# Optimization experiments

Measured on AMD Instinct MI355X. Metric: run time of the kernel, lower is better.

The kernel has to match this reference:

```python
import jax, jax.numpy as jnp
import numpy as np

N, E = 100000, 1600000
DIMS = [128, 64, 64, 64, 32]  # in, hid, hid, hid, out
NEG_SLOPE = 0.2               # GATv2Conv default negative_slope
ELU_ALPHA_OUT = float(DIMS[-1])  # nn.ELU(out_channels): alpha = out_channels


def setup_inputs() -> dict:
    key = jax.random.key(0)
    ks = jax.random.split(key, 16)
    inp = {
        "x": jax.random.normal(ks[0], (N, DIMS[0]), dtype=jnp.float32),
        "edge_index": jax.random.randint(ks[1], (2, E), 0, N, dtype=jnp.int64),
    }
    ki = 2
    for i in range(4):
        fin, fout = DIMS[i], DIMS[i + 1]
        s = 1.0 / np.sqrt(fin)
        inp[f"Wl{i+1}"] = jax.random.uniform(ks[ki], (fin, fout), jnp.float32, -s, s); ki += 1
        inp[f"Wr{i+1}"] = jax.random.uniform(ks[ki], (fin, fout), jnp.float32, -s, s); ki += 1
        inp[f"att{i+1}"] = jax.random.uniform(ks[ki], (fout,), jnp.float32, -s, s); ki += 1
    return inp


def gatv2_layer(x, src, dst, Wl, Wr, att):
    # single head, concat=False, no self-loops, no bias (per module config)
    xl = x @ Wl                                   # [N, F] source-side projection
    xr = x @ Wr                                   # [N, F] target-side projection
    e = jax.nn.leaky_relu(xl[src] + xr[dst], NEG_SLOPE)   # [E, F]
    score = e @ att                               # [E]
    # softmax over incoming edges of each destination node
    m = jax.ops.segment_max(score, dst, num_segments=N)    # [N]
    ex = jnp.exp(score - m[dst])                  # [E]
    denom = jax.ops.segment_sum(ex, dst, num_segments=N)   # [N]
    alpha = ex / (denom[dst] + 1e-16)             # [E]
    # scatter-add weighted source messages
    return jax.ops.segment_sum(xl[src] * alpha[:, None], dst, num_segments=N)


def reference(x, edge_index, Wl1, Wr1, att1, Wl2, Wr2, att2, Wl3, Wr3, att3, Wl4, Wr4, att4):
    src, dst = edge_index[0], edge_index[1]
    h = jax.nn.elu(gatv2_layer(x, src, dst, Wl1, Wr1, att1))
    h = jax.nn.elu(gatv2_layer(h, src, dst, Wl2, Wr2, att2))
    h = jax.nn.elu(gatv2_layer(h, src, dst, Wl3, Wr3, att3))
    h = gatv2_layer(h, src, dst, Wl4, Wr4, att4)
    # nn.ELU(out_channels) -> ELU with alpha = out_channels (faithful quirk)
    return jnp.where(h > 0, h, ELU_ALPHA_OUT * jnp.expm1(h))
```

## Files before the change

### kernel.cpp

```cpp
#include <hip/hip_runtime.h>
#include <math.h>

typedef __attribute__((ext_vector_type(8))) short bf16x8;
typedef __attribute__((ext_vector_type(4))) float f32x4;
typedef __attribute__((ext_vector_type(2))) _Float16 h2;

#define BSHIFT 7
#define CH 8192

__device__ inline unsigned short f32_to_bf16_bits(float f) {
    unsigned int u = __float_as_uint(f);
    unsigned int r = (u + 0x7fffu + ((u >> 16) & 1u)) >> 16;
    return (unsigned short)r;
}
__device__ inline float bf16_bits_to_f32(unsigned short h) {
    return __uint_as_float(((unsigned int)h) << 16);
}
__device__ inline h2 u2h(unsigned u) { return __builtin_bit_cast(h2, u); }
__device__ inline unsigned h2u(h2 h) { return __builtin_bit_cast(unsigned, h); }

#define SWZ_ADD(t, imm) \
    t += __int_as_float(__builtin_amdgcn_ds_swizzle(__float_as_int(t), imm))

__device__ inline float dot2acc(h2 a, h2 b, float c) {
#if defined(__has_builtin)
#if __has_builtin(__builtin_amdgcn_fdot2)
    return __builtin_amdgcn_fdot2(a, b, c, false);
#else
    return c + (float)a[0] * (float)b[0] + (float)a[1] * (float)b[1];
#endif
#else
    return c + (float)a[0] * (float)b[0] + (float)a[1] * (float)b[1];
#endif
}


__global__ __launch_bounds__(256) void bucket_hist(
    const int* __restrict__ dst, int* __restrict__ bcnt8, int E, int nb, int nbp)
{
    __shared__ int h[1024];
    for (int i = threadIdx.x; i < nb; i += 256) h[i] = 0;
    __syncthreads();
    int e0 = blockIdx.x * CH, e1 = min(e0 + CH, E);
    for (int e = e0 + (int)threadIdx.x; e < e1; e += 256)
        atomicAdd(&h[dst[e] >> BSHIFT], 1);
    __syncthreads();
    int* mycnt = bcnt8 + (blockIdx.x & 7) * nbp;
    for (int b = threadIdx.x; b < nb; b += 256) {
        int c = h[b];
        if (c) atomicAdd(&mycnt[b], c);
    }
}

__global__ void bucket_scan(const int* __restrict__ bcnt8, int* __restrict__ bbase,
                            int* __restrict__ bcur8, int* __restrict__ rowstart,
                            int nb, int nbp, int E, int N)
{
    __shared__ int sh[1024];
    int t = threadIdx.x;
    int g8[8];
    int tot = 0;
#pragma unroll
    for (int g = 0; g < 8; ++g) {
        int c = (t < nb) ? bcnt8[g * nbp + t] : 0;
        g8[g] = c; tot += c;
    }
    sh[t] = tot;
    __syncthreads();
    for (int d = 1; d < 1024; d <<= 1) {
        int a = (t >= d) ? sh[t - d] : 0;
        __syncthreads();
        sh[t] += a;
        __syncthreads();
    }
    int base = sh[t] - tot;
    if (t <= nb) bbase[t] = base;
    if (t < nb) {
        int run = base;
#pragma unroll
        for (int g = 0; g < 8; ++g) { bcur8[g * nbp + t] = run; run += g8[g]; }
    }
    if (t == 0) rowstart[N] = E;
}

__global__ __launch_bounds__(256) void bucket_scatter(
    const int* __restrict__ src, const int* __restrict__ dst,
    int* __restrict__ bcur8, unsigned* __restrict__ pairs, int E, int nb, int nbp)
{
    __shared__ int h[1024];
    for (int i = threadIdx.x; i < nb; i += 256) h[i] = 0;
    __syncthreads();
    int e0 = blockIdx.x * CH, e1 = min(e0 + CH, E);
    for (int e = e0 + (int)threadIdx.x; e < e1; e += 256)
        atomicAdd(&h[dst[e] >> BSHIFT], 1);
    __syncthreads();
    int* mycur = bcur8 + (blockIdx.x & 7) * nbp;
    for (int b = threadIdx.x; b < nb; b += 256) {
        int c = h[b];
        if (c) h[b] = atomicAdd(&mycur[b], c);
    }
    __syncthreads();
    for (int e = e0 + (int)threadIdx.x; e < e1; e += 256) {
        int d = dst[e];
        int pos = atomicAdd(&h[d >> BSHIFT], 1);
        pairs[pos] = ((unsigned)src[e] << BSHIFT) | (unsigned)(d & 127);
    }
}

__global__ __launch_bounds__(256) void bucket_finalize(
    const unsigned* __restrict__ pairs, const int* __restrict__ bbase,
    int* __restrict__ rowstart, int* __restrict__ csr_src, int N)
{
    __shared__ int h[128];
    __shared__ int sh[256];
    int b = blockIdx.x;
    int p0 = bbase[b], p1 = bbase[b + 1];
    int t = threadIdx.x;
    if (t < 128) h[t] = 0;
    __syncthreads();
    for (int e = p0 + t; e < p1; e += 256)
        atomicAdd(&h[pairs[e] & 127], 1);
    __syncthreads();
    int v = (t < 128) ? h[t] : 0;
    sh[t] = v;
    __syncthreads();
    for (int d = 1; d < 256; d <<= 1) {
        int a = (t >= d) ? sh[t - d] : 0;
        __syncthreads();
        sh[t] += a;
        __syncthreads();
    }
    if (t < 128) {
        int off = sh[t] - v;
        int node = (b << BSHIFT) + t;
        if (node < N) rowstart[node] = p0 + off;
        h[t] = p0 + off;
    }
    __syncthreads();
    for (int e = p0 + t; e < p1; e += 256) {
        unsigned pr = pairs[e];
        int pos = atomicAdd(&h[pr & 127], 1);
        csr_src[pos] = (int)(pr >> BSHIFT);
    }
}


__global__ void prepack_kernel(const float* __restrict__ Wl, const float* __restrict__ Wr,
                               unsigned short* __restrict__ pWl, unsigned short* __restrict__ pWr,
                               int FIN, int FOUT) {
    int NT = FOUT >> 4, NK = FIN >> 5;
    int part = NT * NK * 512;
    int i = blockIdx.x * blockDim.x + threadIdx.x;
    int m = i / part;
    if (m >= 2) return;
    int ii = i - m * part;
    int j = ii & 7;
    int lane = (ii >> 3) & 63;
    int rest = ii >> 9;
    int ks = rest % NK;
    int t = rest / NK;
    int k = ks * 32 + (lane >> 4) * 8 + j;
    int c = t * 16 + (lane & 15);
    const float* W = m ? Wr : Wl;
    unsigned short* P = m ? pWr : pWl;
    float w = W[(size_t)k * FOUT + c];
    unsigned short hi = f32_to_bf16_bits(w);
    unsigned short lo = f32_to_bf16_bits(w - bf16_bits_to_f32(hi));
    P[ii] = hi;
    P[part + ii] = lo;
}


template<int FIN, int FOUT>
__global__ __launch_bounds__(256) void proj_mfma_kernel(
    const float* __restrict__ x,
    const unsigned short* __restrict__ pWl, const unsigned short* __restrict__ pWr,
    const float* __restrict__ att,
    _Float16* __restrict__ xlh, _Float16* __restrict__ xrh,
    float* __restrict__ dl, float* __restrict__ dr, int n)
{
    constexpr int NT = FOUT >> 4;
    constexpr int NK = FIN >> 5;
    constexpr int PART = NT * NK * 512;
    const int wave = threadIdx.x >> 6;
    const int lane = threadIdx.x & 63;
    const int row0 = blockIdx.x * 64 + wave * 16;
    int arow = row0 + (lane & 15);
    if (arow >= n) arow = n - 1;
    const int khalf = lane >> 4;

    f32x4 accl[NT], accr[NT];
#pragma unroll
    for (int t = 0; t < NT; ++t) {
        accl[t] = (f32x4){0.f, 0.f, 0.f, 0.f};
        accr[t] = (f32x4){0.f, 0.f, 0.f, 0.f};
    }

    const float* xrow = x + (size_t)arow * FIN + khalf * 8;
#pragma unroll
    for (int ks = 0; ks < NK; ++ks) {
        float4 a0 = *(const float4*)(xrow + ks * 32);
        float4 a1 = *(const float4*)(xrow + ks * 32 + 4);
        float av[8] = {a0.x, a0.y, a0.z, a0.w, a1.x, a1.y, a1.z, a1.w};
        bf16x8 ah, al;
#pragma unroll
        for (int j = 0; j < 8; ++j) {
            unsigned short h = f32_to_bf16_bits(av[j]);
            ah[j] = (short)h;
            al[j] = (short)f32_to_bf16_bits(av[j] - bf16_bits_to_f32(h));
        }
#pragma unroll
        for (int t = 0; t < NT; ++t) {
            const unsigned short* bpl = pWl + ((size_t)(t * NK + ks) * 64 + lane) * 8;
            bf16x8 bh  = *(const bf16x8*)bpl;
            bf16x8 blo = *(const bf16x8*)(bpl + PART);
            accl[t] = __builtin_amdgcn_mfma_f32_16x16x32_bf16(ah, bh,  accl[t], 0, 0, 0);
            accl[t] = __builtin_amdgcn_mfma_f32_16x16x32_bf16(ah, blo, accl[t], 0, 0, 0);
            accl[t] = __builtin_amdgcn_mfma_f32_16x16x32_bf16(al, bh,  accl[t], 0, 0, 0);
            const unsigned short* bpr = pWr + ((size_t)(t * NK + ks) * 64 + lane) * 8;
            bh  = *(const bf16x8*)bpr;
            blo = *(const bf16x8*)(bpr + PART);
            accr[t] = __builtin_amdgcn_mfma_f32_16x16x32_bf16(ah, bh,  accr[t], 0, 0, 0);
            accr[t] = __builtin_amdgcn_mfma_f32_16x16x32_bf16(ah, blo, accr[t], 0, 0, 0);
            accr[t] = __builtin_amdgcn_mfma_f32_16x16x32_bf16(al, bh,  accr[t], 0, 0, 0);
        }
    }

    const int orow0 = row0 + khalf * 4;
    const int colb = lane & 15;
    float attc[NT];
#pragma unroll
    for (int t = 0; t < NT; ++t) attc[t] = att[t * 16 + colb];

#pragma unroll
    for (int t = 0; t < NT; ++t) {
        int col = t * 16 + colb;
#pragma unroll
        for (int r = 0; r < 4; ++r) {
            int rr = orow0 + r;
            if (rr < n) {
                xlh[(size_t)rr * FOUT + col] = (_Float16)accl[t][r];
                xrh[(size_t)rr * FOUT + col] = (_Float16)accr[t][r];
            }
        }
    }
#pragma unroll
    for (int r = 0; r < 4; ++r) {
        float pl = 0.f, pr = 0.f;
#pragma unroll
        for (int t = 0; t < NT; ++t) { pl += accl[t][r] * attc[t]; pr += accr[t][r] * attc[t]; }
#pragma unroll
        for (int off = 1; off < 16; off <<= 1) {
            pl += __shfl_xor(pl, off);
            pr += __shfl_xor(pr, off);
        }
        int rr = orow0 + r;
        if (colb == 0 && rr < n) { dl[rr] = pl; dr[rr] = pr; }
    }
}


template<int F, int AMODE>
__global__ __launch_bounds__(256) void agg_kernel(
    const _Float16* __restrict__ xlh, const _Float16* __restrict__ xrh,
    const float* __restrict__ att,
    const float* __restrict__ dl, const float* __restrict__ dr,
    const int* __restrict__ rowstart, const int* __restrict__ csr_src,
    float* __restrict__ out, int n, int E)
{
    constexpr int LPE = F / 8;
    constexpr int LSH = (F == 64) ? 6 : 5;
    constexpr int NPG = 64 / LPE;

    int wv  = (blockIdx.x * blockDim.x + threadIdx.x) >> 6;
    int lane = threadIdx.x & 63;
    int grp = lane / LPE;
    int fl  = lane % LPE;
    int node = wv * NPG + grp;
    bool act = node < n;
    int nc = act ? node : 0;

    float4 xrraw = *(const float4*)(xrh + (((unsigned)nc << LSH) + fl * 8));
    h2 xrv[4];
#pragma unroll
    for (int j = 0; j < 4; ++j) xrv[j] = u2h(((const unsigned*)&xrraw)[j]);
    h2 atth[4];
#pragma unroll
    for (int j = 0; j < 4; ++j) {
        atth[j][0] = (_Float16)att[fl * 8 + 2 * j];
        atth[j][1] = (_Float16)att[fl * 8 + 2 * j + 1];
    }
    float cdr = 0.6f * dr[nc];

    int s0 = rowstart[nc];
    int s1 = act ? rowstart[nc + 1] : s0;
    int s1c = min(max(s1 - 1, s0), E - 1);

    float m = -1e30f, mth = -1e30f, ssum = 0.f;
    float o[8];
#pragma unroll
    for (int j = 0; j < 8; ++j) o[j] = 0.f;

    int cA0 = csr_src[min(s0,     s1c)];
    int cB0 = csr_src[min(s0 + 1, s1c)];
    int cA1 = csr_src[min(s0 + 2, s1c)];
    int cB1 = csr_src[min(s0 + 3, s1c)];
    float4 rA0 = *(const float4*)(xlh + (((unsigned)cA0 << LSH) + fl * 8));
    float4 rB0 = *(const float4*)(xlh + (((unsigned)cB0 << LSH) + fl * 8));
    float  dA0 = dl[cA0], dB0 = dl[cB0];
    float4 rA1 = *(const float4*)(xlh + (((unsigned)cA1 << LSH) + fl * 8));
    float4 rB1 = *(const float4*)(xlh + (((unsigned)cB1 << LSH) + fl * 8));
    float  dA1 = dl[cA1], dB1 = dl[cB1];
    int fA0 = csr_src[min(s0 + 4, s1c)];
    int fB0 = csr_src[min(s0 + 5, s1c)];
    int fA1 = csr_src[min(s0 + 6, s1c)];
    int fB1 = csr_src[min(s0 + 7, s1c)];

    int i0 = s0;

#define AGG_COMPUTE(RA, RB, DA, DB)                                          \
    {                                                                        \
        h2 a[4], b[4];                                                       \
        _Pragma("unroll")                                                    \
        for (int j = 0; j < 4; ++j) {                                        \
            a[j] = u2h(((const unsigned*)&RA)[j]);                           \
            b[j] = u2h(((const unsigned*)&RB)[j]);                           \
        }                                                                    \
        bool vb = (i0 + 1) < s1;                                             \
        float ta = 0.f, tb = 0.f;                                            \
        _Pragma("unroll")                                                    \
        for (int j = 0; j < 4; ++j) {                                        \
            h2 ea = a[j] + xrv[j];                                           \
            h2 eb = b[j] + xrv[j];                                           \
            ea = u2h(h2u(ea) & 0x7FFF7FFFu);                                 \
            eb = u2h(h2u(eb) & 0x7FFF7FFFu);                                 \
            ta = dot2acc(atth[j], ea, ta);                                   \
            tb = dot2acc(atth[j], eb, tb);                                   \
        }                                                                    \
        SWZ_ADD(ta, 0x041F); SWZ_ADD(tb, 0x041F);                            \
        SWZ_ADD(ta, 0x081F); SWZ_ADD(tb, 0x081F);                            \
        if (LPE == 8) { SWZ_ADD(ta, 0x101F); SWZ_ADD(tb, 0x101F); }          \
        float pa = 0.6f * DA + cdr + 0.4f * ta;                              \
        float pb = vb ? (0.6f * DB + cdr + 0.4f * tb) : -1e30f;              \
        float pm = fmaxf(pa, pb);                                            \
        if (pm > mth) {                                                      \
            float c = __expf(m - pm);                                        \
            ssum *= c;                                                       \
            _Pragma("unroll")                                                \
            for (int j = 0; j < 8; ++j) o[j] *= c;                           \
            m = pm; mth = pm + 8.0f;                                         \
        }                                                                    \
        float wa = __expf(pa - m);                                           \
        float wb = __expf(pb - m);                                           \
        ssum += wa + wb;                                                     \
        _Pragma("unroll")                                                    \
        for (int j = 0; j < 4; ++j) {                                        \
            o[2 * j]     += wa * (float)a[j][0] + wb * (float)b[j][0];       \
            o[2 * j + 1] += wa * (float)a[j][1] + wb * (float)b[j][1];       \
        }                                                                    \
    }

    while (i0 < s1) {
        {
            int cA2 = fA0, cB2 = fB0;
            fA0 = csr_src[min(i0 + 8, s1c)];
            fB0 = csr_src[min(i0 + 9, s1c)];
            AGG_COMPUTE(rA0, rB0, dA0, dB0);
            rA0 = *(const float4*)(xlh + (((unsigned)cA2 << LSH) + fl * 8));
            rB0 = *(const float4*)(xlh + (((unsigned)cB2 << LSH) + fl * 8));
            dA0 = dl[cA2]; dB0 = dl[cB2];
        }
        i0 += 2;
        if (i0 >= s1) break;
        {
            int cA2 = fA1, cB2 = fB1;
            fA1 = csr_src[min(i0 + 8, s1c)];
            fB1 = csr_src[min(i0 + 9, s1c)];
            AGG_COMPUTE(rA1, rB1, dA1, dB1);
            rA1 = *(const float4*)(xlh + (((unsigned)cA2 << LSH) + fl * 8));
            rB1 = *(const float4*)(xlh + (((unsigned)cB2 << LSH) + fl * 8));
            dA1 = dl[cA2]; dB1 = dl[cB2];
        }
        i0 += 2;
    }
#undef AGG_COMPUTE

    float inv = 1.f / (ssum + 1e-16f);
    float res[8];
#pragma unroll
    for (int j = 0; j < 8; ++j) {
        float r = o[j] * inv;
        if (AMODE == 1) r = (r > 0.f) ? r : expm1f(r);
        else            r = (r > 0.f) ? r : 32.f * expm1f(r);
        res[j] = r;
    }
    if (act) {
        float* op = out + (((unsigned)node << LSH) + fl * 8);
        *(float4*)op       = (float4){res[0], res[1], res[2], res[3]};
        *(float4*)(op + 4) = (float4){res[4], res[5], res[6], res[7]};
    }
}


extern "C" void kernel_launch(void* const* d_in, const int* in_sizes, int n_in,
                              void* d_out, int out_size, void* d_ws, size_t ws_size,
                              hipStream_t stream) {
    const float* x    = (const float*)d_in[0];
    const int*   ei   = (const int*)d_in[1];
    const float* Wl1  = (const float*)d_in[2];
    const float* Wr1  = (const float*)d_in[3];
    const float* att1 = (const float*)d_in[4];
    const float* Wl2  = (const float*)d_in[5];
    const float* Wr2  = (const float*)d_in[6];
    const float* att2 = (const float*)d_in[7];
    const float* Wl3  = (const float*)d_in[8];
    const float* Wr3  = (const float*)d_in[9];
    const float* att3 = (const float*)d_in[10];
    const float* Wl4  = (const float*)d_in[11];
    const float* Wr4  = (const float*)d_in[12];
    const float* att4 = (const float*)d_in[13];

    const int N = in_sizes[0] / 128;
    const int E = in_sizes[1] / 2;
    const int* src = ei;
    const int* dst = ei + E;

    const int nb  = (N + 127) >> BSHIFT;
    const int nbp = (nb + 15) & ~15;

    char* w = (char*)d_ws;
    size_t off = 0;
    auto take = [&](size_t bytes) -> void* {
        void* p = w + off;
        off = (off + bytes + 255) & ~(size_t)255;
        return p;
    };
    int* bcnt8    = (int*)take((size_t)8 * nbp * 4);
    int* bcur8    = (int*)take((size_t)8 * nbp * 4);
    int* bbase    = (int*)take((size_t)(nb + 1) * 4);
    int* rowstart = (int*)take((size_t)(N + 1) * 4);
    int* csr_src  = (int*)take((size_t)E * 4);
    float* dl = (float*)take((size_t)N * 4);
    float* dr = (float*)take((size_t)N * 4);
    _Float16* xlh = (_Float16*)take((size_t)N * 64 * 2);
    _Float16* xrh = (_Float16*)take((size_t)N * 64 * 2);
    float* hA = (float*)take((size_t)N * 64 * 4);
    float* hB = (float*)take((size_t)N * 64 * 4);
    unsigned short* pWl1 = (unsigned short*)take(2 * 4 * 4 * 512 * 2);
    unsigned short* pWr1 = (unsigned short*)take(2 * 4 * 4 * 512 * 2);
    unsigned short* pWl2 = (unsigned short*)take(2 * 4 * 2 * 512 * 2);
    unsigned short* pWr2 = (unsigned short*)take(2 * 4 * 2 * 512 * 2);
    unsigned short* pWl3 = (unsigned short*)take(2 * 4 * 2 * 512 * 2);
    unsigned short* pWr3 = (unsigned short*)take(2 * 4 * 2 * 512 * 2);
    unsigned short* pWl4 = (unsigned short*)take(2 * 2 * 2 * 512 * 2);
    unsigned short* pWr4 = (unsigned short*)take(2 * 2 * 2 * 512 * 2);
    unsigned* pairs = (unsigned*)hA;
    float* outf = (float*)d_out;

    hipMemsetAsync(bcnt8, 0, (size_t)8 * nbp * 4, stream);

    prepack_kernel<<<(2 * 4 * 4 * 512 + 255) / 256, 256, 0, stream>>>(Wl1, Wr1, pWl1, pWr1, 128, 64);
    prepack_kernel<<<(2 * 4 * 2 * 512 + 255) / 256, 256, 0, stream>>>(Wl2, Wr2, pWl2, pWr2, 64, 64);
    prepack_kernel<<<(2 * 4 * 2 * 512 + 255) / 256, 256, 0, stream>>>(Wl3, Wr3, pWl3, pWr3, 64, 64);
    prepack_kernel<<<(2 * 2 * 2 * 512 + 255) / 256, 256, 0, stream>>>(Wl4, Wr4, pWl4, pWr4, 64, 32);

    int kgrid = (E + CH - 1) / CH;
    bucket_hist<<<kgrid, 256, 0, stream>>>(dst, bcnt8, E, nb, nbp);
    bucket_scan<<<1, 1024, 0, stream>>>(bcnt8, bbase, bcur8, rowstart, nb, nbp, E, N);
    bucket_scatter<<<kgrid, 256, 0, stream>>>(src, dst, bcur8, pairs, E, nb, nbp);
    bucket_finalize<<<nb, 256, 0, stream>>>(pairs, bbase, rowstart, csr_src, N);

    int pblk = (N + 63) / 64;
    int agg64 = (N + 31) / 32;
    int agg32 = (N + 63) / 64;

    proj_mfma_kernel<128, 64><<<pblk, 256, 0, stream>>>(x, pWl1, pWr1, att1, xlh, xrh, dl, dr, N);
    agg_kernel<64, 1><<<agg64, 256, 0, stream>>>(xlh, xrh, att1, dl, dr, rowstart, csr_src, hA, N, E);

    proj_mfma_kernel<64, 64><<<pblk, 256, 0, stream>>>(hA, pWl2, pWr2, att2, xlh, xrh, dl, dr, N);
    agg_kernel<64, 1><<<agg64, 256, 0, stream>>>(xlh, xrh, att2, dl, dr, rowstart, csr_src, hB, N, E);

    proj_mfma_kernel<64, 64><<<pblk, 256, 0, stream>>>(hB, pWl3, pWr3, att3, xlh, xrh, dl, dr, N);
    agg_kernel<64, 1><<<agg64, 256, 0, stream>>>(xlh, xrh, att3, dl, dr, rowstart, csr_src, hA, N, E);

    proj_mfma_kernel<64, 32><<<pblk, 256, 0, stream>>>(hA, pWl4, pWr4, att4, xlh, xrh, dl, dr, N);
    agg_kernel<32, 2><<<agg32, 256, 0, stream>>>(xlh, xrh, att4, dl, dr, rowstart, csr_src, outf, N, E);
}
```

Baseline: 295.5 us.

## Store hidden activations in fp16 and make aggregation grid-stride persistent

Intermediate layer outputs hA/hB are now written as fp16 by the aggregation kernel and read as fp16 by the next projection kernel. This halves activation write and read traffic. The aggregation kernel also becomes a persistent grid-stride loop over node tiles with a fixed grid of 1024 blocks, in place of one wave per tile. The fp16 activations add rounding error, and the persistent loop could change load balance and latency hiding.

```diff
diff --git a/kernel.cpp b/kernel.cpp
--- a/kernel.cpp
+++ b/kernel.cpp
@@ -171,9 +171,9 @@
 }
 
 
-template<int FIN, int FOUT>
+template<int FIN, int FOUT, bool IN16>
 __global__ __launch_bounds__(256) void proj_mfma_kernel(
-    const float* __restrict__ x,
+    const void* __restrict__ xin,
     const unsigned short* __restrict__ pWl, const unsigned short* __restrict__ pWr,
     const float* __restrict__ att,
     _Float16* __restrict__ xlh, _Float16* __restrict__ xrh,
@@ -196,12 +196,26 @@
         accr[t] = (f32x4){0.f, 0.f, 0.f, 0.f};
     }
 
-    const float* xrow = x + (size_t)arow * FIN + khalf * 8;
 #pragma unroll
     for (int ks = 0; ks < NK; ++ks) {
-        float4 a0 = *(const float4*)(xrow + ks * 32);
-        float4 a1 = *(const float4*)(xrow + ks * 32 + 4);
-        float av[8] = {a0.x, a0.y, a0.z, a0.w, a1.x, a1.y, a1.z, a1.w};
+        float av[8];
+        if (IN16) {
+            const _Float16* xrow = (const _Float16*)xin + (size_t)arow * FIN + khalf * 8;
+            float4 raw = *(const float4*)(xrow + ks * 32);
+            const unsigned* u = (const unsigned*)&raw;
+#pragma unroll
+            for (int j = 0; j < 4; ++j) {
+                h2 p = u2h(u[j]);
+                av[2 * j]     = (float)p[0];
+                av[2 * j + 1] = (float)p[1];
+            }
+        } else {
+            const float* xrow = (const float*)xin + (size_t)arow * FIN + khalf * 8;
+            float4 a0 = *(const float4*)(xrow + ks * 32);
+            float4 a1 = *(const float4*)(xrow + ks * 32 + 4);
+            av[0] = a0.x; av[1] = a0.y; av[2] = a0.z; av[3] = a0.w;
+            av[4] = a1.x; av[5] = a1.y; av[6] = a1.z; av[7] = a1.w;
+        }
         bf16x8 ah, al;
 #pragma unroll
         for (int j = 0; j < 8; ++j) {
@@ -260,144 +274,162 @@
 }
 
 
-template<int F, int AMODE>
+template<int F, int AMODE, bool OUT16>
 __global__ __launch_bounds__(256) void agg_kernel(
     const _Float16* __restrict__ xlh, const _Float16* __restrict__ xrh,
     const float* __restrict__ att,
     const float* __restrict__ dl, const float* __restrict__ dr,
     const int* __restrict__ rowstart, const int* __restrict__ csr_src,
-    float* __restrict__ out, int n, int E)
+    void* __restrict__ outv, int n, int E, int ntiles)
 {
     constexpr int LPE = F / 8;
     constexpr int LSH = (F == 64) ? 6 : 5;
     constexpr int NPG = 64 / LPE;
 
-    int wv  = (blockIdx.x * blockDim.x + threadIdx.x) >> 6;
+    int wv0  = (blockIdx.x * blockDim.x + threadIdx.x) >> 6;
+    int nwaves = gridDim.x * (blockDim.x >> 6);
     int lane = threadIdx.x & 63;
     int grp = lane / LPE;
     int fl  = lane % LPE;
-    int node = wv * NPG + grp;
-    bool act = node < n;
-    int nc = act ? node : 0;
-
-    float4 xrraw = *(const float4*)(xrh + (((unsigned)nc << LSH) + fl * 8));
-    h2 xrv[4];
-#pragma unroll
-    for (int j = 0; j < 4; ++j) xrv[j] = u2h(((const unsigned*)&xrraw)[j]);
+
     h2 atth[4];
 #pragma unroll
     for (int j = 0; j < 4; ++j) {
         atth[j][0] = (_Float16)att[fl * 8 + 2 * j];
         atth[j][1] = (_Float16)att[fl * 8 + 2 * j + 1];
     }
-    float cdr = 0.6f * dr[nc];
-
-    int s0 = rowstart[nc];
-    int s1 = act ? rowstart[nc + 1] : s0;
-    int s1c = min(max(s1 - 1, s0), E - 1);
-
-    float m = -1e30f, mth = -1e30f, ssum = 0.f;
-    float o[8];
-#pragma unroll
-    for (int j = 0; j < 8; ++j) o[j] = 0.f;
-
-    int cA0 = csr_src[min(s0,     s1c)];
-    int cB0 = csr_src[min(s0 + 1, s1c)];
-    int cA1 = csr_src[min(s0 + 2, s1c)];
-    int cB1 = csr_src[min(s0 + 3, s1c)];
-    float4 rA0 = *(const float4*)(xlh + (((unsigned)cA0 << LSH) + fl * 8));
-    float4 rB0 = *(const float4*)(xlh + (((unsigned)cB0 << LSH) + fl * 8));
-    float  dA0 = dl[cA0], dB0 = dl[cB0];
-    float4 rA1 = *(const float4*)(xlh + (((unsigned)cA1 << LSH) + fl * 8));
-    float4 rB1 = *(const float4*)(xlh + (((unsigned)cB1 << LSH) + fl * 8));
-    float  dA1 = dl[cA1], dB1 = dl[cB1];
-    int fA0 = csr_src[min(s0 + 4, s1c)];
-    int fB0 = csr_src[min(s0 + 5, s1c)];
-    int fA1 = csr_src[min(s0 + 6, s1c)];
-    int fB1 = csr_src[min(s0 + 7, s1c)];
-
-    int i0 = s0;
+
+    for (int tile = wv0; tile < ntiles; tile += nwaves) {
+        int node = tile * NPG + grp;
+        bool act = node < n;
+        int nc = act ? node : 0;
+
+        float4 xrraw = *(const float4*)(xrh + (((unsigned)nc << LSH) + fl * 8));
+        h2 xrv[4];
+#pragma unroll
+        for (int j = 0; j < 4; ++j) xrv[j] = u2h(((const unsigned*)&xrraw)[j]);
+        float cdr = 0.6f * dr[nc];
+
+        int s0 = rowstart[nc];
+        int s1 = act ? rowstart[nc + 1] : s0;
+        int s1c = min(max(s1 - 1, s0), E - 1);
+
+        float m = -1e30f, mth = -1e30f, ssum = 0.f;
+        float o[8];
+#pragma unroll
+        for (int j = 0; j < 8; ++j) o[j] = 0.f;
+
+        int cA0 = csr_src[min(s0,     s1c)];
+        int cB0 = csr_src[min(s0 + 1, s1c)];
+        int cA1 = csr_src[min(s0 + 2, s1c)];
+        int cB1 = csr_src[min(s0 + 3, s1c)];
+        float4 rA0 = *(const float4*)(xlh + (((unsigned)cA0 << LSH) + fl * 8));
+        float4 rB0 = *(const float4*)(xlh + (((unsigned)cB0 << LSH) + fl * 8));
+        float  dA0 = dl[cA0], dB0 = dl[cB0];
+        float4 rA1 = *(const float4*)(xlh + (((unsigned)cA1 << LSH) + fl * 8));
+        float4 rB1 = *(const float4*)(xlh + (((unsigned)cB1 << LSH) + fl * 8));
+        float  dA1 = dl[cA1], dB1 = dl[cB1];
+        int fA0 = csr_src[min(s0 + 4, s1c)];
+        int fB0 = csr_src[min(s0 + 5, s1c)];
+        int fA1 = csr_src[min(s0 + 6, s1c)];
+        int fB1 = csr_src[min(s0 + 7, s1c)];
+
+        int i0 = s0;
 
 #define AGG_COMPUTE(RA, RB, DA, DB)                                          \
-    {                                                                        \
-        h2 a[4], b[4];                                                       \
-        _Pragma("unroll")                                                    \
-        for (int j = 0; j < 4; ++j) {                                        \
-            a[j] = u2h(((const unsigned*)&RA)[j]);                           \
-            b[j] = u2h(((const unsigned*)&RB)[j]);                           \
-        }                                                                    \
-        bool vb = (i0 + 1) < s1;                                             \
-        float ta = 0.f, tb = 0.f;                                            \
-        _Pragma("unroll")                                                    \
-        for (int j = 0; j < 4; ++j) {                                        \
-            h2 ea = a[j] + xrv[j];                                           \
-            h2 eb = b[j] + xrv[j];                                           \
-            ea = u2h(h2u(ea) & 0x7FFF7FFFu);                                 \
-            eb = u2h(h2u(eb) & 0x7FFF7FFFu);                                 \
-            ta = dot2acc(atth[j], ea, ta);                                   \
-            tb = dot2acc(atth[j], eb, tb);                                   \
-        }                                                                    \
-        SWZ_ADD(ta, 0x041F); SWZ_ADD(tb, 0x041F);                            \
-        SWZ_ADD(ta, 0x081F); SWZ_ADD(tb, 0x081F);                            \
-        if (LPE == 8) { SWZ_ADD(ta, 0x101F); SWZ_ADD(tb, 0x101F); }          \
-        float pa = 0.6f * DA + cdr + 0.4f * ta;                              \
-        float pb = vb ? (0.6f * DB + cdr + 0.4f * tb) : -1e30f;              \
-        float pm = fmaxf(pa, pb);                                            \
-        if (pm > mth) {                                                      \
-            float c = __expf(m - pm);                                        \
-            ssum *= c;                                                       \
+        {                                                                    \
+            h2 a[4], b[4];                                                   \
             _Pragma("unroll")                                                \
-            for (int j = 0; j < 8; ++j) o[j] *= c;                           \
-            m = pm; mth = pm + 8.0f;                                         \
-        }                                                                    \
-        float wa = __expf(pa - m);                                           \
-        float wb = __expf(pb - m);                                           \
-        ssum += wa + wb;                                                     \
-        _Pragma("unroll")                                                    \
-        for (int j = 0; j < 4; ++j) {                                        \
-            o[2 * j]     += wa * (float)a[j][0] + wb * (float)b[j][0];       \
-            o[2 * j + 1] += wa * (float)a[j][1] + wb * (float)b[j][1];       \
-        }                                                                    \
-    }
-
-    while (i0 < s1) {
-        {
-            int cA2 = fA0, cB2 = fB0;
-            fA0 = csr_src[min(i0 + 8, s1c)];
-            fB0 = csr_src[min(i0 + 9, s1c)];
-            AGG_COMPUTE(rA0, rB0, dA0, dB0);
-            rA0 = *(const float4*)(xlh + (((unsigned)cA2 << LSH) + fl * 8));
-            rB0 = *(const float4*)(xlh + (((unsigned)cB2 << LSH) + fl * 8));
-            dA0 = dl[cA2]; dB0 = dl[cB2];
-        }
-        i0 += 2;
-        if (i0 >= s1) break;
-        {
-            int cA2 = fA1, cB2 = fB1;
-            fA1 = csr_src[min(i0 + 8, s1c)];
-            fB1 = csr_src[min(i0 + 9, s1c)];
-            AGG_COMPUTE(rA1, rB1, dA1, dB1);
-            rA1 = *(const float4*)(xlh + (((unsigned)cA2 << LSH) + fl * 8));
-            rB1 = *(const float4*)(xlh + (((unsigned)cB2 << LSH) + fl * 8));
-            dA1 = dl[cA2]; dB1 = dl[cB2];
-        }
-        i0 += 2;
-    }
+            for (int j = 0; j < 4; ++j) {                                    \
+                a[j] = u2h(((const unsigned*)&RA)[j]);                       \
+                b[j] = u2h(((const unsigned*)&RB)[j]);                       \
+            }                                                                \
+            bool vb = (i0 + 1) < s1;                                         \
+            float ta = 0.f, tb = 0.f;                                        \
+            _Pragma("unroll")                                                \
+            for (int j = 0; j < 4; ++j) {                                    \
+                h2 ea = a[j] + xrv[j];                                       \
+                h2 eb = b[j] + xrv[j];                                       \
+                ea = u2h(h2u(ea) & 0x7FFF7FFFu);                             \
+                eb = u2h(h2u(eb) & 0x7FFF7FFFu);                             \
+                ta = dot2acc(atth[j], ea, ta);                               \
+                tb = dot2acc(atth[j], eb, tb);                               \
+            }                                                                \
+            SWZ_ADD(ta, 0x041F); SWZ_ADD(tb, 0x041F);                        \
+            SWZ_ADD(ta, 0x081F); SWZ_ADD(tb, 0x081F);                        \
+            if (LPE == 8) { SWZ_ADD(ta, 0x101F); SWZ_ADD(tb, 0x101F); }      \
+            float pa = 0.6f * DA + cdr + 0.4f * ta;                          \
+            float pb = vb ? (0.6f * DB + cdr + 0.4f * tb) : -1e30f;          \
+            float pm = fmaxf(pa, pb);                                        \
+            if (pm > mth) {                                                  \
+                float c = __expf(m - pm);                                    \
+                ssum *= c;                                                   \
+                _Pragma("unroll")                                            \
+                for (int j = 0; j < 8; ++j) o[j] *= c;                       \
+                m = pm; mth = pm + 8.0f;                                     \
+            }                                                                \
+            float wa = __expf(pa - m);                                       \
+            float wb = __expf(pb - m);                                       \
+            ssum += wa + wb;                                                 \
+            _Pragma("unroll")                                                \
+            for (int j = 0; j < 4; ++j) {                                    \
+                o[2 * j]     += wa * (float)a[j][0] + wb * (float)b[j][0];   \
+                o[2 * j + 1] += wa * (float)a[j][1] + wb * (float)b[j][1];   \
+            }                                                                \
+        }
+
+        while (i0 < s1) {
+            {
+                int cA2 = fA0, cB2 = fB0;
+                fA0 = csr_src[min(i0 + 8, s1c)];
+                fB0 = csr_src[min(i0 + 9, s1c)];
+                AGG_COMPUTE(rA0, rB0, dA0, dB0);
+                rA0 = *(const float4*)(xlh + (((unsigned)cA2 << LSH) + fl * 8));
+                rB0 = *(const float4*)(xlh + (((unsigned)cB2 << LSH) + fl * 8));
+                dA0 = dl[cA2]; dB0 = dl[cB2];
+            }
+            i0 += 2;
+            if (i0 >= s1) break;
+            {
+                int cA2 = fA1, cB2 = fB1;
+                fA1 = csr_src[min(i0 + 8, s1c)];
+                fB1 = csr_src[min(i0 + 9, s1c)];
+                AGG_COMPUTE(rA1, rB1, dA1, dB1);
+                rA1 = *(const float4*)(xlh + (((unsigned)cA2 << LSH) + fl * 8));
+                rB1 = *(const float4*)(xlh + (((unsigned)cB2 << LSH) + fl * 8));
+                dA1 = dl[cA2]; dB1 = dl[cB2];
+            }
+            i0 += 2;
+        }
 #undef AGG_COMPUTE
 
-    float inv = 1.f / (ssum + 1e-16f);
-    float res[8];
-#pragma unroll
-    for (int j = 0; j < 8; ++j) {
-        float r = o[j] * inv;
-        if (AMODE == 1) r = (r > 0.f) ? r : expm1f(r);
-        else            r = (r > 0.f) ? r : 32.f * expm1f(r);
-        res[j] = r;
-    }
-    if (act) {
-        float* op = out + (((unsigned)node << LSH) + fl * 8);
-        *(float4*)op       = (float4){res[0], res[1], res[2], res[3]};
-        *(float4*)(op + 4) = (float4){res[4], res[5], res[6], res[7]};
+        float inv = 1.f / (ssum + 1e-16f);
+        float res[8];
+#pragma unroll
+        for (int j = 0; j < 8; ++j) {
+            float r = o[j] * inv;
+            if (AMODE == 1) r = (r > 0.f) ? r : expm1f(r);
+            else            r = (r > 0.f) ? r : 32.f * expm1f(r);
+            res[j] = r;
+        }
+        if (act) {
+            if (OUT16) {
+                unsigned pk[4];
+#pragma unroll
+                for (int j = 0; j < 4; ++j) {
+                    h2 t;
+                    t[0] = (_Float16)res[2 * j];
+                    t[1] = (_Float16)res[2 * j + 1];
+                    pk[j] = h2u(t);
+                }
+                _Float16* op = (_Float16*)outv + (((unsigned)node << LSH) + fl * 8);
+                *(float4*)op = *(const float4*)pk;
+            } else {
+                float* op = (float*)outv + (((unsigned)node << LSH) + fl * 8);
+                *(float4*)op       = (float4){res[0], res[1], res[2], res[3]};
+                *(float4*)(op + 4) = (float4){res[4], res[5], res[6], res[7]};
+            }
+        }
     }
 }
 
@@ -444,8 +476,8 @@
     float* dr = (float*)take((size_t)N * 4);
     _Float16* xlh = (_Float16*)take((size_t)N * 64 * 2);
     _Float16* xrh = (_Float16*)take((size_t)N * 64 * 2);
-    float* hA = (float*)take((size_t)N * 64 * 4);
-    float* hB = (float*)take((size_t)N * 64 * 4);
+    _Float16* hA  = (_Float16*)take((size_t)N * 64 * 2);
+    _Float16* hB  = (_Float16*)take((size_t)N * 64 * 2);
     unsigned short* pWl1 = (unsigned short*)take(2 * 4 * 4 * 512 * 2);
     unsigned short* pWr1 = (unsigned short*)take(2 * 4 * 4 * 512 * 2);
     unsigned short* pWl2 = (unsigned short*)take(2 * 4 * 2 * 512 * 2);
@@ -471,18 +503,19 @@
     bucket_finalize<<<nb, 256, 0, stream>>>(pairs, bbase, rowstart, csr_src, N);
 
     int pblk = (N + 63) / 64;
-    int agg64 = (N + 31) / 32;
-    int agg32 = (N + 63) / 64;
-
-    proj_mfma_kernel<128, 64><<<pblk, 256, 0, stream>>>(x, pWl1, pWr1, att1, xlh, xrh, dl, dr, N);
-    agg_kernel<64, 1><<<agg64, 256, 0, stream>>>(xlh, xrh, att1, dl, dr, rowstart, csr_src, hA, N, E);
-
-    proj_mfma_kernel<64, 64><<<pblk, 256, 0, stream>>>(hA, pWl2, pWr2, att2, xlh, xrh, dl, dr, N);
-    agg_kernel<64, 1><<<agg64, 256, 0, stream>>>(xlh, xrh, att2, dl, dr, rowstart, csr_src, hB, N, E);
-
-    proj_mfma_kernel<64, 64><<<pblk, 256, 0, stream>>>(hB, pWl3, pWr3, att3, xlh, xrh, dl, dr, N);
-    agg_kernel<64, 1><<<agg64, 256, 0, stream>>>(xlh, xrh, att3, dl, dr, rowstart, csr_src, hA, N, E);
-
-    proj_mfma_kernel<64, 32><<<pblk, 256, 0, stream>>>(hA, pWl4, pWr4, att4, xlh, xrh, dl, dr, N);
-    agg_kernel<32, 2><<<agg32, 256, 0, stream>>>(xlh, xrh, att4, dl, dr, rowstart, csr_src, outf, N, E);
-}
+    const int AGGB = 1024;
+    int nt64 = (N + 7) / 8;
+    int nt32 = (N + 15) / 16;
+
+    proj_mfma_kernel<128, 64, false><<<pblk, 256, 0, stream>>>(x, pWl1, pWr1, att1, xlh, xrh, dl, dr, N);
+    agg_kernel<64, 1, true><<<AGGB, 256, 0, stream>>>(xlh, xrh, att1, dl, dr, rowstart, csr_src, hA, N, E, nt64);
+
+    proj_mfma_kernel<64, 64, true><<<pblk, 256, 0, stream>>>(hA, pWl2, pWr2, att2, xlh, xrh, dl, dr, N);
+    agg_kernel<64, 1, true><<<AGGB, 256, 0, stream>>>(xlh, xrh, att2, dl, dr, rowstart, csr_src, hB, N, E, nt64);
+
+    proj_mfma_kernel<64, 64, true><<<pblk, 256, 0, stream>>>(hB, pWl3, pWr3, att3, xlh, xrh, dl, dr, N);
+    agg_kernel<64, 1, true><<<AGGB, 256, 0, stream>>>(xlh, xrh, att3, dl, dr, rowstart, csr_src, hA, N, E, nt64);
+
+    proj_mfma_kernel<64, 32, true><<<pblk, 256, 0, stream>>>(hA, pWl4, pWr4, att4, xlh, xrh, dl, dr, N);
+    agg_kernel<32, 2, false><<<AGGB, 256, 0, stream>>>(xlh, xrh, att4, dl, dr, rowstart, csr_src, outf, N, E, nt32);
+}
```

After: 308.5 us. 4.4% more time.
